# Kernel optimization log

Hardware: AMD Instinct MI355X
Metric: run time of the kernel (lower is better)

Reference implementation:

```python
import jax, jax.numpy as jnp
import numpy as np

N = 50000          # total points (25 clouds x 2000 pts)
C = 64             # feature channels (in == out, no bottleneck)
K_NN = 16          # neighbors kept per dilation branch
DILATIONS = (1, 2, 4)
KMAX = K_NN * max(DILATIONS)   # base kNN graph has k*d_max neighbors per node
B = 25             # number of point clouds
EPS = 1e-16


def setup_inputs() -> dict:
    key = jax.random.key(0)
    ks = jax.random.split(key, 8)
    x = jax.random.normal(ks[0], (N, C), jnp.float32)
    pos = jax.random.normal(ks[1], (N, 3), jnp.float32)
    # kNN-style edge_index [2, N*KMAX]: row0 = source/neighbor j, row1 = center i,
    # KMAX consecutive edges per center node, neighbors restricted to the same cloud.
    pts = N // B
    cloud_base = (jnp.arange(N) // pts) * pts
    src = cloud_base[:, None] + jax.random.randint(ks[2], (N, KMAX), 0, pts)
    dst = jnp.broadcast_to(jnp.arange(N)[:, None], (N, KMAX))
    edge_index = jnp.stack([src.reshape(-1), dst.reshape(-1)]).astype(jnp.int32)
    batch = jnp.repeat(jnp.arange(B), pts).astype(jnp.int32)
    nD = len(DILATIONS)
    s = 1.0 / np.sqrt(C)
    Wv = jax.random.normal(ks[3], (nD, C, C), jnp.float32) * s   # lin (value)
    Wq = jax.random.normal(ks[4], (nD, C, C), jnp.float32) * s   # lin_dst
    Wk = jax.random.normal(ks[5], (nD, C, C), jnp.float32) * s   # lin_src
    Wp = jax.random.normal(ks[6], (nD, 3, C), jnp.float32) * (1.0 / np.sqrt(3.0))  # pos_nn
    bp = jax.random.normal(ks[7], (nD, C), jnp.float32) * 0.01
    return dict(x=x, pos=pos, Wv=Wv, Wq=Wq, Wk=Wk, Wp=Wp, bp=bp,
                edge_index=edge_index, batch=batch)


def _dilated_edges(edge_index, k, d):
    # take every d-th of the first k*d neighbors within each node's block -> k edges/node
    e = edge_index.reshape(2, -1, KMAX)[:, :, : k * d : d]
    return e.reshape(2, -1)


def _segment_softmax(a, seg, n):
    amax = jax.ops.segment_max(a, seg, num_segments=n)
    e = jnp.exp(a - amax[seg])
    s = jax.ops.segment_sum(e, seg, num_segments=n)
    return e / (s[seg] + EPS)


def _pt_conv(x, pos, src, dst, Wv, Wq, Wk, Wp, bp):
    # PyG PointTransformerConv: msg = softmax_i(q_i - k_j + delta_ij) * (v_j + delta_ij)
    n = x.shape[0]
    q = x @ Wq        # [N, C]  (lin_dst)
    kk = x @ Wk       # [N, C]  (lin_src)
    v = x @ Wv        # [N, C]  (lin, value)
    delta = (pos[dst] - pos[src]) @ Wp + bp            # [E, C] positional encoding
    alpha = _segment_softmax(q[dst] - kk[src] + delta, dst, n)
    return jax.ops.segment_sum(alpha * (v[src] + delta), dst, num_segments=n)


def reference(x, pos, Wv, Wq, Wk, Wp, bp, edge_index, batch):
    inputs = x
    res = None
    for i, d in enumerate(DILATIONS):
        e = _dilated_edges(edge_index, K_NN, d)
        h = _pt_conv(x, pos, e[0], e[1], Wv[i], Wq[i], Wk[i], Wp[i], bp[i])
        res = h if res is None else jnp.maximum(res, h)   # stack+max over branches
    # global max pool per cloud, gathered back per node
    pool = jax.ops.segment_max(x, batch, num_segments=B)[batch]
    res = jnp.maximum(res, pool)
    return res + inputs   # residual
```

## Files before the change

### kernel.cpp

```cpp
#include <hip/hip_runtime.h>
#include <math.h>

#define NP 50000
#define CH 64
#define KMAX 64
#define KNN 16
#define NB 25
#define PTS (NP / NB)
#define EPSF 1e-16f
#define NTILES (NP / 16)
#define ATILES (NP / 4)
#define L2E 1.4426950408889634f
#define LN2 0.6931471805599453f
#define PPB 8
#define PROWS (PTS / PPB)

typedef __attribute__((ext_vector_type(8))) short short8;
typedef __attribute__((ext_vector_type(4))) float float4v;
typedef __attribute__((ext_vector_type(4))) unsigned int uint4v;
typedef __attribute__((ext_vector_type(2))) unsigned int uint2v;
typedef __attribute__((ext_vector_type(4))) unsigned short ushort4v;

__device__ __forceinline__ ushort f2b(float f) {
  unsigned u = __float_as_uint(f);
  unsigned r = (u + 0x7FFFu + ((u >> 16) & 1u)) >> 16;
  return (ushort)r;
}
__device__ __forceinline__ float b2f(ushort h) {
  return __uint_as_float(((unsigned)h) << 16);
}

#define QBF_BYTES   ((size_t)3 * NP * CH * 2)
#define KVP_BYTES   ((size_t)3 * NP * CH * 4)
#define XBF_BYTES   ((size_t)NP * CH * 2)
#define WPACK_ELEMS (9 * 4 * 2 * 64 * 8)
#define XV (NP * CH / 4)

__global__ __launch_bounds__(256) void prep_kernel(
    const float* __restrict__ x,
    const float* __restrict__ Wv,
    const float* __restrict__ Wq,
    const float* __restrict__ Wk,
    ushort* __restrict__ x_bf,
    ushort* __restrict__ wpack,
    float* __restrict__ poolP) {
  const int tid = threadIdx.x;
  const int bid = blockIdx.x;
  __shared__ float red[4][CH];

  if (bid < NB * PPB) {
    const int lane = tid & 63;
    const int wave = tid >> 6;
    const int cloud = bid >> 3;
    const int part  = bid & 7;
    const float* xb = x + ((size_t)cloud * PTS + part * PROWS) * CH;
    float m0 = -INFINITY, m1 = -INFINITY;
    for (int r = wave * 2; r < PROWS; r += 8) {
      m0 = fmaxf(m0, xb[(size_t)(r + 0) * CH + lane]);
      m1 = fmaxf(m1, xb[(size_t)(r + 1) * CH + lane]);
    }
    red[wave][lane] = fmaxf(m0, m1);
    __syncthreads();
    if (wave == 0) {
      poolP[(size_t)bid * CH + lane] = fmaxf(fmaxf(red[0][lane], red[1][lane]),
                                             fmaxf(red[2][lane], red[3][lane]));
    }
  } else {
    const int gid = (bid - NB * PPB) * 256 + tid;
    if (gid < XV) {
      const float4* xv = (const float4*)x;
      float4 v = xv[gid];
      ushort4v o;
      o[0] = f2b(v.x); o[1] = f2b(v.y); o[2] = f2b(v.z); o[3] = f2b(v.w);
      *(ushort4v*)(x_bf + (size_t)gid * 4) = o;
    } else {
      int pid = gid - XV;
      if (pid < WPACK_ELEMS) {
        int j     = pid & 7;
        int lane  = (pid >> 3) & 63;
        int kstep = (pid >> 9) & 1;
        int mtile = (pid >> 10) & 3;
        int mat   = pid >> 12;
        const float* W;
        int d;
        float scale;
        if (mat < 3)      { W = Wq; d = mat;     scale = L2E; }
        else if (mat < 6) { W = Wk; d = mat - 3; scale = L2E; }
        else              { W = Wv; d = mat - 6; scale = 1.f; }
        int oc = mtile * 16 + (lane & 15);
        int ic = kstep * 32 + ((lane >> 4) & 3) * 8 + j;
        wpack[pid] = f2b(W[d * CH * CH + ic * CH + oc] * scale);
      }
    }
  }
}

__global__ __launch_bounds__(256) void qkv_mfma(
    const ushort* __restrict__ x_bf,
    const ushort* __restrict__ wpack,
    ushort* __restrict__ qbf,
    unsigned int* __restrict__ kvp) {
  const int lane = threadIdx.x;
  const int tile = blockIdx.x * 4 + threadIdx.y;
  if (tile >= NTILES) return;
  const int y = blockIdx.y;
  const int kbase = (lane >> 4) * 8;
  const int myNode = tile * 16 + (lane & 15);
  const ushort* xr = x_bf + (size_t)myNode * CH;
  short8 b0 = *(const short8*)(xr + kbase);
  short8 b1 = *(const short8*)(xr + 32 + kbase);

  if (y < 3) {
    const int dd = y;
    ushort* outQ = qbf + (size_t)dd * NP * CH;
#pragma unroll
    for (int mt = 0; mt < 4; ++mt) {
      short8 a0 = *(const short8*)(wpack +
          ((((size_t)dd * 4 + mt) * 2 + 0) * 64 + lane) * 8);
      short8 a1 = *(const short8*)(wpack +
          ((((size_t)dd * 4 + mt) * 2 + 1) * 64 + lane) * 8);
      float4v acc = {0.f, 0.f, 0.f, 0.f};
      acc = __builtin_amdgcn_mfma_f32_16x16x32_bf16(a0, b0, acc, 0, 0, 0);
      acc = __builtin_amdgcn_mfma_f32_16x16x32_bf16(a1, b1, acc, 0, 0, 0);
      int oc = mt * 16 + (lane >> 4) * 4;
      uint2v o;
      o[0] = (unsigned)f2b(acc[0]) | ((unsigned)f2b(acc[1]) << 16);
      o[1] = (unsigned)f2b(acc[2]) | ((unsigned)f2b(acc[3]) << 16);
      *(uint2v*)(outQ + (size_t)myNode * CH + oc) = o;
    }
  } else {
    const int dd = y - 3;
    unsigned int* outKV = kvp + (size_t)dd * NP * CH;
#pragma unroll
    for (int mt = 0; mt < 4; ++mt) {
      short8 k0 = *(const short8*)(wpack +
          ((((size_t)(3 + dd) * 4 + mt) * 2 + 0) * 64 + lane) * 8);
      short8 k1 = *(const short8*)(wpack +
          ((((size_t)(3 + dd) * 4 + mt) * 2 + 1) * 64 + lane) * 8);
      short8 v0 = *(const short8*)(wpack +
          ((((size_t)(6 + dd) * 4 + mt) * 2 + 0) * 64 + lane) * 8);
      short8 v1 = *(const short8*)(wpack +
          ((((size_t)(6 + dd) * 4 + mt) * 2 + 1) * 64 + lane) * 8);
      float4v aK = {0.f, 0.f, 0.f, 0.f};
      float4v aV = {0.f, 0.f, 0.f, 0.f};
      aK = __builtin_amdgcn_mfma_f32_16x16x32_bf16(k0, b0, aK, 0, 0, 0);
      aK = __builtin_amdgcn_mfma_f32_16x16x32_bf16(k1, b1, aK, 0, 0, 0);
      aV = __builtin_amdgcn_mfma_f32_16x16x32_bf16(v0, b0, aV, 0, 0, 0);
      aV = __builtin_amdgcn_mfma_f32_16x16x32_bf16(v1, b1, aV, 0, 0, 0);
      int oc = mt * 16 + (lane >> 4) * 4;
      uint4v o;
#pragma unroll
      for (int i = 0; i < 4; ++i)
        o[i] = ((unsigned)f2b(aK[i]) << 16) | (unsigned)f2b(aV[i]);
      *(uint4v*)(outKV + (size_t)myNode * CH + oc) = o;
    }
  }
}

__global__ __launch_bounds__(384, 6) void attn_kernel(
    const float* __restrict__ x,
    const float* __restrict__ pos,
    const float* __restrict__ Wp,
    const float* __restrict__ bp,
    const int*   __restrict__ edge_src,
    const ushort* __restrict__ qbf,
    const unsigned int* __restrict__ kvp,
    const float* __restrict__ poolP,
    float* __restrict__ out) {
  const int bx  = blockIdx.x;
  const int xcd = bx & 7;
  const int kk  = bx >> 3;
  const int base = (ATILES * xcd) >> 3;
  const int cnt  = ((ATILES * (xcd + 1)) >> 3) - base;
  if (kk >= cnt) return;
  const int node0 = (base + kk) * 4;

  const int wy   = threadIdx.y;
  const int dd   = wy % 3;
  const int half = wy / 3;
  const int tid  = wy * 64 + threadIdx.x;

  __shared__ float sEdge[4 * 260];
  __shared__ float sS[6 * 4 * 68];
  __shared__ float sP[6 * 4 * 68];

  if (tid < 256) {
    int nl = tid >> 6, p = tid & 63;
    int nd = node0 + nl;
    int j = edge_src[(size_t)nd * KMAX + p];
    float4v w;
    w[0] = pos[nd * 3 + 0] - pos[j * 3 + 0];
    w[1] = pos[nd * 3 + 1] - pos[j * 3 + 1];
    w[2] = pos[nd * 3 + 2] - pos[j * 3 + 2];
    w[3] = __int_as_float(j << 8);
    *(float4v*)&sEdge[nl * 260 + p * 4] = w;
  }
  __syncthreads();

  const int lane = threadIdx.x;
  const int g    = lane >> 4;
  const int cl   = lane & 15;
  const int node = node0 + g;
  const unsigned clOfs = (unsigned)(cl << 4);

  float4v bq, qorig, wp0, wp1, wp2;
  {
    ushort4v qh = *(const ushort4v*)(qbf + ((size_t)dd * NP + node) * CH + cl * 4);
    const float* WpD = Wp + dd * 192;
    wp0 = *(const float4v*)(WpD + 0 * 64 + cl * 4) * L2E;
    wp1 = *(const float4v*)(WpD + 1 * 64 + cl * 4) * L2E;
    wp2 = *(const float4v*)(WpD + 2 * 64 + cl * 4) * L2E;
    float4v bpv = *(const float4v*)(bp + dd * 64 + cl * 4);
    float4v qf;
#pragma unroll
    for (int i = 0; i < 4; ++i) qf[i] = b2f(qh[i]);
    bq = qf + bpv * L2E;
    qorig = qf * LN2;
  }
  const char* KVb = (const char*)(kvp + (size_t)dd * NP * CH);

  const float* ep = &sEdge[g * 260] + (((half * 8) << dd) * 4);
  const int estep = (1 << dd) * 4;

  float4v s    = {0.f, 0.f, 0.f, 0.f};
  float4v accv = {0.f, 0.f, 0.f, 0.f};
#pragma unroll
  for (int e = 0; e < 8; ++e) {
    float4v w = *(const float4v*)ep;
    ep += estep;
    uint4v u = *(const uint4v*)(KVb + (__float_as_uint(w[3]) + clOfs));
    float4v kf, vf, wgt;
#pragma unroll
    for (int i = 0; i < 4; ++i) kf[i] = __uint_as_float(u[i] & 0xFFFF0000u);
#pragma unroll
    for (int i = 0; i < 4; ++i) vf[i] = __uint_as_float(u[i] << 16);
    float4v t = bq + w[0] * wp0 + w[1] * wp1 + w[2] * wp2;
    float4v a = t - kf;
#pragma unroll
    for (int i = 0; i < 4; ++i) wgt[i] = __builtin_amdgcn_exp2f(a[i]);
    s += wgt;
    accv += wgt * (vf + t * LN2);
  }

  float4v P = accv - qorig * s;
  *(float4v*)&sS[(wy * 4 + g) * 68 + cl * 4] = s;
  *(float4v*)&sP[(wy * 4 + g) * 68 + cl * 4] = P;
  __syncthreads();

  if (wy == 0) {
    float4v res;
#pragma unroll
    for (int d2 = 0; d2 < 3; ++d2) {
      float4v s0 = *(const float4v*)&sS[((d2    ) * 4 + g) * 68 + cl * 4];
      float4v s1 = *(const float4v*)&sS[((d2 + 3) * 4 + g) * 68 + cl * 4];
      float4v p0 = *(const float4v*)&sP[((d2    ) * 4 + g) * 68 + cl * 4];
      float4v p1 = *(const float4v*)&sP[((d2 + 3) * 4 + g) * 68 + cl * 4];
      float4v st = s0 + s1;
      float4v pt = p0 + p1;
      float4v r;
#pragma unroll
      for (int i = 0; i < 4; ++i)
        r[i] = pt[i] * __builtin_amdgcn_rcpf(st[i] + EPSF);
      if (d2 == 0) res = r;
      else {
#pragma unroll
        for (int i = 0; i < 4; ++i) res[i] = fmaxf(res[i], r[i]);
      }
    }
    const int b = node / PTS;
    const float* pp = poolP + (size_t)(b * PPB) * CH + cl * 4;
    float4v pv = *(const float4v*)pp;
#pragma unroll
    for (int q2 = 1; q2 < PPB; ++q2) {
      float4v t2 = *(const float4v*)(pp + (size_t)q2 * CH);
#pragma unroll
      for (int i = 0; i < 4; ++i) pv[i] = fmaxf(pv[i], t2[i]);
    }
    float4v xv = *(const float4v*)(x + (size_t)node * CH + cl * 4);
#pragma unroll
    for (int i = 0; i < 4; ++i) res[i] = fmaxf(res[i], pv[i]) + xv[i];
    *(float4v*)(out + (size_t)node * CH + cl * 4) = res;
  }
}

extern "C" void kernel_launch(void* const* d_in, const int* in_sizes, int n_in,
                              void* d_out, int out_size, void* d_ws, size_t ws_size,
                              hipStream_t stream) {
  const float* x    = (const float*)d_in[0];
  const float* pos  = (const float*)d_in[1];
  const float* Wv   = (const float*)d_in[2];
  const float* Wq   = (const float*)d_in[3];
  const float* Wk   = (const float*)d_in[4];
  const float* Wp   = (const float*)d_in[5];
  const float* bp   = (const float*)d_in[6];
  const int*   ei   = (const int*)d_in[7];
  float* out = (float*)d_out;

  char* wsb = (char*)d_ws;
  ushort* qbf   = (ushort*)wsb;
  unsigned int* kvp = (unsigned int*)(wsb + QBF_BYTES);
  ushort* x_bf  = (ushort*)(wsb + QBF_BYTES + KVP_BYTES);
  ushort* wpack = (ushort*)(wsb + QBF_BYTES + KVP_BYTES + XBF_BYTES);
  float*  poolP = (float*)(wsb + QBF_BYTES + KVP_BYTES + XBF_BYTES +
                           (size_t)WPACK_ELEMS * 2);

  {
    int convBlocks = (XV + WPACK_ELEMS + 255) / 256;
    dim3 grid(NB * PPB + convBlocks);
    hipLaunchKernelGGL(prep_kernel, grid, dim3(256), 0, stream,
                       x, Wv, Wq, Wk, x_bf, wpack, poolP);
  }
  {
    dim3 grid((NTILES + 3) / 4, 6);
    dim3 block(64, 4);
    hipLaunchKernelGGL(qkv_mfma, grid, block, 0, stream, x_bf, wpack, qbf, kvp);
  }
  {
    dim3 grid(8 * ((ATILES + 7) / 8));
    dim3 block(64, 6);
    hipLaunchKernelGGL(attn_kernel, grid, block, 0, stream,
                       x, pos, Wp, bp, ei, qbf, kvp, poolP, out);
  }
}
```

Baseline: 186.7 us.

## Process eight nodes per attention block with two interleaved node streams per wave

The attention kernel now handles 8 nodes per block instead of 4, so each lane runs two independent neighbor-accumulation chains (nodes A and B) interleaved in the edge loop. This gives more memory-level parallelism for the gathered K/V loads and halves the block count and per-block setup. Two waves now do the final reduction instead of one. The cost is higher register pressure and larger shared memory per block, which under launch_bounds(384,6) may cause spills or lower occupancy. The key unpack also drops the mask on the high bf16 half, leaving the low value bits in the mantissa as a small precision change.

```diff
diff --git a/kernel.cpp b/kernel.cpp
--- a/kernel.cpp
+++ b/kernel.cpp
@@ -9,7 +9,7 @@
 #define PTS (NP / NB)
 #define EPSF 1e-16f
 #define NTILES (NP / 16)
-#define ATILES (NP / 4)
+#define OCTS (NP / 8)
 #define L2E 1.4426950408889634f
 #define LN2 0.6931471805599453f
 #define PPB 8
@@ -170,22 +170,22 @@
   const int bx  = blockIdx.x;
   const int xcd = bx & 7;
   const int kk  = bx >> 3;
-  const int base = (ATILES * xcd) >> 3;
-  const int cnt  = ((ATILES * (xcd + 1)) >> 3) - base;
+  const int base = (OCTS * xcd) >> 3;
+  const int cnt  = ((OCTS * (xcd + 1)) >> 3) - base;
   if (kk >= cnt) return;
-  const int node0 = (base + kk) * 4;
+  const int node0 = (base + kk) * 8;
 
   const int wy   = threadIdx.y;
   const int dd   = wy % 3;
   const int half = wy / 3;
   const int tid  = wy * 64 + threadIdx.x;
 
-  __shared__ float sEdge[4 * 260];
-  __shared__ float sS[6 * 4 * 68];
-  __shared__ float sP[6 * 4 * 68];
-
-  if (tid < 256) {
-    int nl = tid >> 6, p = tid & 63;
+  __shared__ float sEdge[8 * 260];
+  __shared__ float sS[6 * 8 * 68];
+  __shared__ float sP[6 * 8 * 68];
+
+  for (int r = tid; r < 8 * KMAX; r += 384) {
+    int nl = r >> 6, p = r & 63;
     int nd = node0 + nl;
     int j = edge_src[(size_t)nd * KMAX + p];
     float4v w;
@@ -200,61 +200,82 @@
   const int lane = threadIdx.x;
   const int g    = lane >> 4;
   const int cl   = lane & 15;
-  const int node = node0 + g;
+  const int nodeA = node0 + g;
+  const int nodeB = node0 + 4 + g;
   const unsigned clOfs = (unsigned)(cl << 4);
 
-  float4v bq, qorig, wp0, wp1, wp2;
-  {
-    ushort4v qh = *(const ushort4v*)(qbf + ((size_t)dd * NP + node) * CH + cl * 4);
+  float4v wp0, wp1, wp2, bpv, bqA, bqB;
+  {
     const float* WpD = Wp + dd * 192;
     wp0 = *(const float4v*)(WpD + 0 * 64 + cl * 4) * L2E;
     wp1 = *(const float4v*)(WpD + 1 * 64 + cl * 4) * L2E;
     wp2 = *(const float4v*)(WpD + 2 * 64 + cl * 4) * L2E;
-    float4v bpv = *(const float4v*)(bp + dd * 64 + cl * 4);
-    float4v qf;
-#pragma unroll
-    for (int i = 0; i < 4; ++i) qf[i] = b2f(qh[i]);
-    bq = qf + bpv * L2E;
-    qorig = qf * LN2;
+    bpv = *(const float4v*)(bp + dd * 64 + cl * 4) * L2E;
+    ushort4v qA = *(const ushort4v*)(qbf + ((size_t)dd * NP + nodeA) * CH + cl * 4);
+    ushort4v qB = *(const ushort4v*)(qbf + ((size_t)dd * NP + nodeB) * CH + cl * 4);
+#pragma unroll
+    for (int i = 0; i < 4; ++i) {
+      bqA[i] = b2f(qA[i]) + bpv[i];
+      bqB[i] = b2f(qB[i]) + bpv[i];
+    }
   }
   const char* KVb = (const char*)(kvp + (size_t)dd * NP * CH);
 
-  const float* ep = &sEdge[g * 260] + (((half * 8) << dd) * 4);
-  const int estep = (1 << dd) * 4;
-
-  float4v s    = {0.f, 0.f, 0.f, 0.f};
-  float4v accv = {0.f, 0.f, 0.f, 0.f};
+  const int e0   = (half * 8) << dd;
+  const int estp = (1 << dd) * 4;
+  const float* epA = &sEdge[g * 260] + e0 * 4;
+  const float* epB = &sEdge[(4 + g) * 260] + e0 * 4;
+
+  float4v sA = {0.f, 0.f, 0.f, 0.f}, accA = {0.f, 0.f, 0.f, 0.f};
+  float4v sB = {0.f, 0.f, 0.f, 0.f}, accB = {0.f, 0.f, 0.f, 0.f};
 #pragma unroll
   for (int e = 0; e < 8; ++e) {
-    float4v w = *(const float4v*)ep;
-    ep += estep;
-    uint4v u = *(const uint4v*)(KVb + (__float_as_uint(w[3]) + clOfs));
-    float4v kf, vf, wgt;
-#pragma unroll
-    for (int i = 0; i < 4; ++i) kf[i] = __uint_as_float(u[i] & 0xFFFF0000u);
-#pragma unroll
-    for (int i = 0; i < 4; ++i) vf[i] = __uint_as_float(u[i] << 16);
-    float4v t = bq + w[0] * wp0 + w[1] * wp1 + w[2] * wp2;
-    float4v a = t - kf;
-#pragma unroll
-    for (int i = 0; i < 4; ++i) wgt[i] = __builtin_amdgcn_exp2f(a[i]);
-    s += wgt;
-    accv += wgt * (vf + t * LN2);
-  }
-
-  float4v P = accv - qorig * s;
-  *(float4v*)&sS[(wy * 4 + g) * 68 + cl * 4] = s;
-  *(float4v*)&sP[(wy * 4 + g) * 68 + cl * 4] = P;
+    float4v wA = *(const float4v*)(epA + e * estp);
+    float4v wB = *(const float4v*)(epB + e * estp);
+    uint4v uA = *(const uint4v*)(KVb + (__float_as_uint(wA[3]) + clOfs));
+    uint4v uB = *(const uint4v*)(KVb + (__float_as_uint(wB[3]) + clOfs));
+    float4v tA = bqA + wA[0] * wp0 + wA[1] * wp1 + wA[2] * wp2;
+    float4v tB = bqB + wB[0] * wp0 + wB[1] * wp1 + wB[2] * wp2;
+    float4v gA, gB;
+#pragma unroll
+    for (int i = 0; i < 4; ++i) {
+      gA[i] = __builtin_amdgcn_exp2f(tA[i] - __uint_as_float(uA[i]));
+      gB[i] = __builtin_amdgcn_exp2f(tB[i] - __uint_as_float(uB[i]));
+    }
+    float4v vA, vB;
+#pragma unroll
+    for (int i = 0; i < 4; ++i) {
+      vA[i] = __uint_as_float(uA[i] << 16);
+      vB[i] = __uint_as_float(uB[i] << 16);
+    }
+    sA += gA;  accA += gA * (vA + tA * LN2);
+    sB += gB;  accB += gB * (vB + tB * LN2);
+  }
+
+  {
+    float4v qoA, qoB;
+#pragma unroll
+    for (int i = 0; i < 4; ++i) {
+      qoA[i] = (bqA[i] - bpv[i]) * LN2;
+      qoB[i] = (bqB[i] - bpv[i]) * LN2;
+    }
+    *(float4v*)&sS[(wy * 8 + g) * 68 + cl * 4]     = sA;
+    *(float4v*)&sP[(wy * 8 + g) * 68 + cl * 4]     = accA - qoA * sA;
+    *(float4v*)&sS[(wy * 8 + 4 + g) * 68 + cl * 4] = sB;
+    *(float4v*)&sP[(wy * 8 + 4 + g) * 68 + cl * 4] = accB - qoB * sB;
+  }
   __syncthreads();
 
-  if (wy == 0) {
+  if (wy < 2) {
+    const int g2 = wy * 4 + g;
+    const int node = node0 + g2;
     float4v res;
 #pragma unroll
     for (int d2 = 0; d2 < 3; ++d2) {
-      float4v s0 = *(const float4v*)&sS[((d2    ) * 4 + g) * 68 + cl * 4];
-      float4v s1 = *(const float4v*)&sS[((d2 + 3) * 4 + g) * 68 + cl * 4];
-      float4v p0 = *(const float4v*)&sP[((d2    ) * 4 + g) * 68 + cl * 4];
-      float4v p1 = *(const float4v*)&sP[((d2 + 3) * 4 + g) * 68 + cl * 4];
+      float4v s0 = *(const float4v*)&sS[((d2    ) * 8 + g2) * 68 + cl * 4];
+      float4v s1 = *(const float4v*)&sS[((d2 + 3) * 8 + g2) * 68 + cl * 4];
+      float4v p0 = *(const float4v*)&sP[((d2    ) * 8 + g2) * 68 + cl * 4];
+      float4v p1 = *(const float4v*)&sP[((d2 + 3) * 8 + g2) * 68 + cl * 4];
       float4v st = s0 + s1;
       float4v pt = p0 + p1;
       float4v r;
@@ -316,7 +337,7 @@
     hipLaunchKernelGGL(qkv_mfma, grid, block, 0, stream, x_bf, wpack, qbf, kvp);
   }
   {
-    dim3 grid(8 * ((ATILES + 7) / 8));
+    dim3 grid(8 * ((OCTS + 7) / 8));
     dim3 block(64, 6);
     hipLaunchKernelGGL(attn_kernel, grid, block, 0, stream,
                        x, pos, Wp, bp, ei, qbf, kvp, poolP, out);
```

Result: slower. 639.5 us (+242.5%).

## Fuse bf16 conversion of x into QKV MFMA kernel and batch gathers in attention

Applied to the files above, without the earlier changes.

The separate x-to-bf16 conversion pass and its workspace buffer are removed. The QKV kernel now loads fp32 x tiles into shared memory, converts them there, and one 6-wave block computes all Q/K/V branches with weights held in registers across 4 tiles. This cuts a global write and re-read of x_bf and reloads of the packed weights. The attention inner loop now issues four KV gathers before computing, to raise memory-level parallelism, and uses fma forms and a cheaper k extraction. This costs more registers and LDS per block.

```diff
diff --git a/kernel.cpp b/kernel.cpp
--- a/kernel.cpp
+++ b/kernel.cpp
@@ -9,11 +9,12 @@
 #define PTS (NP / NB)
 #define EPSF 1e-16f
 #define NTILES (NP / 16)
-#define ATILES (NP / 4)
+#define OCTS (NP / 4)
 #define L2E 1.4426950408889634f
 #define LN2 0.6931471805599453f
 #define PPB 8
 #define PROWS (PTS / PPB)
+#define TPB 4
 
 typedef __attribute__((ext_vector_type(8))) short short8;
 typedef __attribute__((ext_vector_type(4))) float float4v;
@@ -32,16 +33,13 @@
 
 #define QBF_BYTES   ((size_t)3 * NP * CH * 2)
 #define KVP_BYTES   ((size_t)3 * NP * CH * 4)
-#define XBF_BYTES   ((size_t)NP * CH * 2)
 #define WPACK_ELEMS (9 * 4 * 2 * 64 * 8)
-#define XV (NP * CH / 4)
 
 __global__ __launch_bounds__(256) void prep_kernel(
     const float* __restrict__ x,
     const float* __restrict__ Wv,
     const float* __restrict__ Wq,
     const float* __restrict__ Wk,
-    ushort* __restrict__ x_bf,
     ushort* __restrict__ wpack,
     float* __restrict__ poolP) {
   const int tid = threadIdx.x;
@@ -66,93 +64,112 @@
                                              fmaxf(red[2][lane], red[3][lane]));
     }
   } else {
-    const int gid = (bid - NB * PPB) * 256 + tid;
-    if (gid < XV) {
-      const float4* xv = (const float4*)x;
-      float4 v = xv[gid];
-      ushort4v o;
-      o[0] = f2b(v.x); o[1] = f2b(v.y); o[2] = f2b(v.z); o[3] = f2b(v.w);
-      *(ushort4v*)(x_bf + (size_t)gid * 4) = o;
-    } else {
-      int pid = gid - XV;
-      if (pid < WPACK_ELEMS) {
-        int j     = pid & 7;
-        int lane  = (pid >> 3) & 63;
-        int kstep = (pid >> 9) & 1;
-        int mtile = (pid >> 10) & 3;
-        int mat   = pid >> 12;
-        const float* W;
-        int d;
-        float scale;
-        if (mat < 3)      { W = Wq; d = mat;     scale = L2E; }
-        else if (mat < 6) { W = Wk; d = mat - 3; scale = L2E; }
-        else              { W = Wv; d = mat - 6; scale = 1.f; }
-        int oc = mtile * 16 + (lane & 15);
-        int ic = kstep * 32 + ((lane >> 4) & 3) * 8 + j;
-        wpack[pid] = f2b(W[d * CH * CH + ic * CH + oc] * scale);
-      }
-    }
-  }
-}
-
-__global__ __launch_bounds__(256) void qkv_mfma(
-    const ushort* __restrict__ x_bf,
+    int pid = (bid - NB * PPB) * 256 + tid;
+    if (pid < WPACK_ELEMS) {
+      int j     = pid & 7;
+      int lane  = (pid >> 3) & 63;
+      int kstep = (pid >> 9) & 1;
+      int mtile = (pid >> 10) & 3;
+      int mat   = pid >> 12;
+      const float* W;
+      int d;
+      float scale;
+      if (mat < 3)      { W = Wq; d = mat;     scale = L2E; }
+      else if (mat < 6) { W = Wk; d = mat - 3; scale = L2E; }
+      else              { W = Wv; d = mat - 6; scale = 1.f; }
+      int oc = mtile * 16 + (lane & 15);
+      int ic = kstep * 32 + ((lane >> 4) & 3) * 8 + j;
+      wpack[pid] = f2b(W[d * CH * CH + ic * CH + oc] * scale);
+    }
+  }
+}
+
+__global__ __launch_bounds__(384, 2) void qkv_fused(
+    const float* __restrict__ x,
     const ushort* __restrict__ wpack,
     ushort* __restrict__ qbf,
     unsigned int* __restrict__ kvp) {
+  const int t0 = blockIdx.x * TPB;
+  const int count = (NTILES - t0 < TPB) ? (NTILES - t0) : TPB;
+  const int tid = threadIdx.y * 64 + threadIdx.x;
+
+  __shared__ ushort xs[TPB][16][72];
+
+  for (int g = tid; g < count * 256; g += 384) {
+    float4 v = ((const float4*)x)[(size_t)t0 * 256 + g];
+    int tile = g >> 8;
+    int rem  = g & 255;
+    int node = rem >> 4;
+    int c4   = rem & 15;
+    ushort4v o;
+    o[0] = f2b(v.x); o[1] = f2b(v.y); o[2] = f2b(v.z); o[3] = f2b(v.w);
+    *(ushort4v*)&xs[tile][node][c4 * 4] = o;
+  }
+  __syncthreads();
+
   const int lane = threadIdx.x;
-  const int tile = blockIdx.x * 4 + threadIdx.y;
-  if (tile >= NTILES) return;
-  const int y = blockIdx.y;
+  const int y    = threadIdx.y;
   const int kbase = (lane >> 4) * 8;
-  const int myNode = tile * 16 + (lane & 15);
-  const ushort* xr = x_bf + (size_t)myNode * CH;
-  short8 b0 = *(const short8*)(xr + kbase);
-  short8 b1 = *(const short8*)(xr + 32 + kbase);
+  const int nl    = lane & 15;
 
   if (y < 3) {
     const int dd = y;
+    short8 af[4][2];
+#pragma unroll
+    for (int mt = 0; mt < 4; ++mt)
+#pragma unroll
+      for (int ks = 0; ks < 2; ++ks)
+        af[mt][ks] = *(const short8*)(wpack +
+            ((((size_t)dd * 4 + mt) * 2 + ks) * 64 + lane) * 8);
     ushort* outQ = qbf + (size_t)dd * NP * CH;
-#pragma unroll
-    for (int mt = 0; mt < 4; ++mt) {
-      short8 a0 = *(const short8*)(wpack +
-          ((((size_t)dd * 4 + mt) * 2 + 0) * 64 + lane) * 8);
-      short8 a1 = *(const short8*)(wpack +
-          ((((size_t)dd * 4 + mt) * 2 + 1) * 64 + lane) * 8);
-      float4v acc = {0.f, 0.f, 0.f, 0.f};
-      acc = __builtin_amdgcn_mfma_f32_16x16x32_bf16(a0, b0, acc, 0, 0, 0);
-      acc = __builtin_amdgcn_mfma_f32_16x16x32_bf16(a1, b1, acc, 0, 0, 0);
-      int oc = mt * 16 + (lane >> 4) * 4;
-      uint2v o;
-      o[0] = (unsigned)f2b(acc[0]) | ((unsigned)f2b(acc[1]) << 16);
-      o[1] = (unsigned)f2b(acc[2]) | ((unsigned)f2b(acc[3]) << 16);
-      *(uint2v*)(outQ + (size_t)myNode * CH + oc) = o;
+    for (int t = 0; t < count; ++t) {
+      short8 b0 = *(const short8*)&xs[t][nl][kbase];
+      short8 b1 = *(const short8*)&xs[t][nl][kbase + 32];
+      int myNode = (t0 + t) * 16 + nl;
+#pragma unroll
+      for (int mt = 0; mt < 4; ++mt) {
+        float4v acc = {0.f, 0.f, 0.f, 0.f};
+        acc = __builtin_amdgcn_mfma_f32_16x16x32_bf16(af[mt][0], b0, acc, 0, 0, 0);
+        acc = __builtin_amdgcn_mfma_f32_16x16x32_bf16(af[mt][1], b1, acc, 0, 0, 0);
+        int oc = mt * 16 + (lane >> 4) * 4;
+        uint2v o;
+        o[0] = (unsigned)f2b(acc[0]) | ((unsigned)f2b(acc[1]) << 16);
+        o[1] = (unsigned)f2b(acc[2]) | ((unsigned)f2b(acc[3]) << 16);
+        *(uint2v*)(outQ + (size_t)myNode * CH + oc) = o;
+      }
     }
   } else {
     const int dd = y - 3;
+    short8 afK[4][2], afV[4][2];
+#pragma unroll
+    for (int mt = 0; mt < 4; ++mt)
+#pragma unroll
+      for (int ks = 0; ks < 2; ++ks) {
+        afK[mt][ks] = *(const short8*)(wpack +
+            ((((size_t)(3 + dd) * 4 + mt) * 2 + ks) * 64 + lane) * 8);
+        afV[mt][ks] = *(const short8*)(wpack +
+            ((((size_t)(6 + dd) * 4 + mt) * 2 + ks) * 64 + lane) * 8);
+      }
     unsigned int* outKV = kvp + (size_t)dd * NP * CH;
-#pragma unroll
-    for (int mt = 0; mt < 4; ++mt) {
-      short8 k0 = *(const short8*)(wpack +
-          ((((size_t)(3 + dd) * 4 + mt) * 2 + 0) * 64 + lane) * 8);
-      short8 k1 = *(const short8*)(wpack +
-          ((((size_t)(3 + dd) * 4 + mt) * 2 + 1) * 64 + lane) * 8);
-      short8 v0 = *(const short8*)(wpack +
-          ((((size_t)(6 + dd) * 4 + mt) * 2 + 0) * 64 + lane) * 8);
-      short8 v1 = *(const short8*)(wpack +
-          ((((size_t)(6 + dd) * 4 + mt) * 2 + 1) * 64 + lane) * 8);
-      float4v aK = {0.f, 0.f, 0.f, 0.f};
-      float4v aV = {0.f, 0.f, 0.f, 0.f};
-      aK = __builtin_amdgcn_mfma_f32_16x16x32_bf16(k0, b0, aK, 0, 0, 0);
-      aK = __builtin_amdgcn_mfma_f32_16x16x32_bf16(k1, b1, aK, 0, 0, 0);
-      aV = __builtin_amdgcn_mfma_f32_16x16x32_bf16(v0, b0, aV, 0, 0, 0);
-      aV = __builtin_amdgcn_mfma_f32_16x16x32_bf16(v1, b1, aV, 0, 0, 0);
-      int oc = mt * 16 + (lane >> 4) * 4;
-      uint4v o;
-#pragma unroll
-      for (int i = 0; i < 4; ++i)
-        o[i] = ((unsigned)f2b(aK[i]) << 16) | (unsigned)f2b(aV[i]);
-      *(uint4v*)(outKV + (size_t)myNode * CH + oc) = o;
+    for (int t = 0; t < count; ++t) {
+      short8 b0 = *(const short8*)&xs[t][nl][kbase];
+      short8 b1 = *(const short8*)&xs[t][nl][kbase + 32];
+      int myNode = (t0 + t) * 16 + nl;
+#pragma unroll
+      for (int mt = 0; mt < 4; ++mt) {
+        float4v aK = {0.f, 0.f, 0.f, 0.f};
+        float4v aV = {0.f, 0.f, 0.f, 0.f};
+        aK = __builtin_amdgcn_mfma_f32_16x16x32_bf16(afK[mt][0], b0, aK, 0, 0, 0);
+        aK = __builtin_amdgcn_mfma_f32_16x16x32_bf16(afK[mt][1], b1, aK, 0, 0, 0);
+        aV = __builtin_amdgcn_mfma_f32_16x16x32_bf16(afV[mt][0], b0, aV, 0, 0, 0);
+        aV = __builtin_amdgcn_mfma_f32_16x16x32_bf16(afV[mt][1], b1, aV, 0, 0, 0);
+        int oc = mt * 16 + (lane >> 4) * 4;
+        uint4v o;
+#pragma unroll
+        for (int i = 0; i < 4; ++i)
+          o[i] = ((unsigned)f2b(aK[i]) << 16) | (unsigned)f2b(aV[i]);
+        *(uint4v*)(outKV + (size_t)myNode * CH + oc) = o;
+      }
     }
   }
 }
@@ -170,8 +187,8 @@
   const int bx  = blockIdx.x;
   const int xcd = bx & 7;
   const int kk  = bx >> 3;
-  const int base = (ATILES * xcd) >> 3;
-  const int cnt  = ((ATILES * (xcd + 1)) >> 3) - base;
+  const int base = (OCTS * xcd) >> 3;
+  const int cnt  = ((OCTS * (xcd + 1)) >> 3) - base;
   if (kk >= cnt) return;
   const int node0 = (base + kk) * 4;
 
@@ -203,48 +220,57 @@
   const int node = node0 + g;
   const unsigned clOfs = (unsigned)(cl << 4);
 
-  float4v bq, qorig, wp0, wp1, wp2;
+  float4v bq, bpv, wp0, wp1, wp2;
   {
     ushort4v qh = *(const ushort4v*)(qbf + ((size_t)dd * NP + node) * CH + cl * 4);
     const float* WpD = Wp + dd * 192;
     wp0 = *(const float4v*)(WpD + 0 * 64 + cl * 4) * L2E;
     wp1 = *(const float4v*)(WpD + 1 * 64 + cl * 4) * L2E;
     wp2 = *(const float4v*)(WpD + 2 * 64 + cl * 4) * L2E;
-    float4v bpv = *(const float4v*)(bp + dd * 64 + cl * 4);
-    float4v qf;
-#pragma unroll
-    for (int i = 0; i < 4; ++i) qf[i] = b2f(qh[i]);
-    bq = qf + bpv * L2E;
-    qorig = qf * LN2;
+    bpv = *(const float4v*)(bp + dd * 64 + cl * 4) * L2E;
+#pragma unroll
+    for (int i = 0; i < 4; ++i) bq[i] = b2f(qh[i]) + bpv[i];
   }
   const char* KVb = (const char*)(kvp + (size_t)dd * NP * CH);
 
-  const float* ep = &sEdge[g * 260] + (((half * 8) << dd) * 4);
-  const int estep = (1 << dd) * 4;
+  const float* sMy = &sEdge[g * 260] + (((half * 8) << dd) * 4);
+  const int estp = (1 << dd) * 4;
 
   float4v s    = {0.f, 0.f, 0.f, 0.f};
   float4v accv = {0.f, 0.f, 0.f, 0.f};
 #pragma unroll
-  for (int e = 0; e < 8; ++e) {
-    float4v w = *(const float4v*)ep;
-    ep += estep;
-    uint4v u = *(const uint4v*)(KVb + (__float_as_uint(w[3]) + clOfs));
-    float4v kf, vf, wgt;
-#pragma unroll
-    for (int i = 0; i < 4; ++i) kf[i] = __uint_as_float(u[i] & 0xFFFF0000u);
-#pragma unroll
-    for (int i = 0; i < 4; ++i) vf[i] = __uint_as_float(u[i] << 16);
-    float4v t = bq + w[0] * wp0 + w[1] * wp1 + w[2] * wp2;
-    float4v a = t - kf;
-#pragma unroll
-    for (int i = 0; i < 4; ++i) wgt[i] = __builtin_amdgcn_exp2f(a[i]);
-    s += wgt;
-    accv += wgt * (vf + t * LN2);
-  }
-
-  float4v P = accv - qorig * s;
-  *(float4v*)&sS[(wy * 4 + g) * 68 + cl * 4] = s;
-  *(float4v*)&sP[(wy * 4 + g) * 68 + cl * 4] = P;
+  for (int b4 = 0; b4 < 2; ++b4) {
+    float4v w4[4];
+    uint4v  u4[4];
+#pragma unroll
+    for (int j = 0; j < 4; ++j)
+      w4[j] = *(const float4v*)(sMy + (b4 * 4 + j) * estp);
+#pragma unroll
+    for (int j = 0; j < 4; ++j)
+      u4[j] = *(const uint4v*)(KVb + (__float_as_uint(w4[j][3]) + clOfs));
+#pragma unroll
+    for (int j = 0; j < 4; ++j) {
+      float4v t = bq + w4[j][0] * wp0 + w4[j][1] * wp1 + w4[j][2] * wp2;
+      float4v wgt, vf;
+#pragma unroll
+      for (int i = 0; i < 4; ++i) {
+        wgt[i] = __builtin_amdgcn_exp2f(t[i] - __uint_as_float(u4[j][i]));
+        vf[i]  = __uint_as_float(u4[j][i] << 16);
+      }
+      s += wgt;
+#pragma unroll
+      for (int i = 0; i < 4; ++i)
+        accv[i] = fmaf(wgt[i], fmaf(LN2, t[i], vf[i]), accv[i]);
+    }
+  }
+
+  {
+    float4v qo;
+#pragma unroll
+    for (int i = 0; i < 4; ++i) qo[i] = (bq[i] - bpv[i]) * LN2;
+    *(float4v*)&sS[(wy * 4 + g) * 68 + cl * 4] = s;
+    *(float4v*)&sP[(wy * 4 + g) * 68 + cl * 4] = accv - qo * s;
+  }
   __syncthreads();
 
   if (wy == 0) {
@@ -299,24 +325,22 @@
   char* wsb = (char*)d_ws;
   ushort* qbf   = (ushort*)wsb;
   unsigned int* kvp = (unsigned int*)(wsb + QBF_BYTES);
-  ushort* x_bf  = (ushort*)(wsb + QBF_BYTES + KVP_BYTES);
-  ushort* wpack = (ushort*)(wsb + QBF_BYTES + KVP_BYTES + XBF_BYTES);
-  float*  poolP = (float*)(wsb + QBF_BYTES + KVP_BYTES + XBF_BYTES +
-                           (size_t)WPACK_ELEMS * 2);
-
-  {
-    int convBlocks = (XV + WPACK_ELEMS + 255) / 256;
-    dim3 grid(NB * PPB + convBlocks);
+  ushort* wpack = (ushort*)(wsb + QBF_BYTES + KVP_BYTES);
+  float*  poolP = (float*)(wsb + QBF_BYTES + KVP_BYTES + (size_t)WPACK_ELEMS * 2);
+
+  {
+    int packBlocks = (WPACK_ELEMS + 255) / 256;
+    dim3 grid(NB * PPB + packBlocks);
     hipLaunchKernelGGL(prep_kernel, grid, dim3(256), 0, stream,
-                       x, Wv, Wq, Wk, x_bf, wpack, poolP);
-  }
-  {
-    dim3 grid((NTILES + 3) / 4, 6);
-    dim3 block(64, 4);
-    hipLaunchKernelGGL(qkv_mfma, grid, block, 0, stream, x_bf, wpack, qbf, kvp);
-  }
-  {
-    dim3 grid(8 * ((ATILES + 7) / 8));
+                       x, Wv, Wq, Wk, wpack, poolP);
+  }
+  {
+    dim3 grid((NTILES + TPB - 1) / TPB);
+    dim3 block(64, 6);
+    hipLaunchKernelGGL(qkv_fused, grid, block, 0, stream, x, wpack, qbf, kvp);
+  }
+  {
+    dim3 grid(8 * ((OCTS + 7) / 8));
     dim3 block(64, 6);
     hipLaunchKernelGGL(attn_kernel, grid, block, 0, stream,
                        x, pos, Wp, bp, ei, qbf, kvp, poolP, out);
```

Measured after the change: 395.5 us. +111.8%, slower.
